# Kernel optimization log

Measured on AMD Instinct MI355X. Metric: run time of the kernel, lower is better.

Reference implementation:

```python
import jax, jax.numpy as jnp
import numpy as np

B, S, D, H = 2, 2048, 1024, 16
DK = D // H

def setup_inputs() -> dict:
    key = jax.random.key(0)
    ks = jax.random.split(key, 11)
    scale = 0.02
    inp = {
        "Q": jax.random.normal(ks[0], (B, S, D), jnp.float32),
        "K": jax.random.normal(ks[1], (B, S, D), jnp.float32),
        "V": jax.random.normal(ks[2], (B, S, D), jnp.float32),
        "mask": jnp.ones((B, S), jnp.int32),
        "Wq": jax.random.normal(ks[3], (D, D), jnp.float32) * scale,
        "bq": jnp.zeros((D,), jnp.float32),
        "Wk": jax.random.normal(ks[4], (D, D), jnp.float32) * scale,
        "bk": jnp.zeros((D,), jnp.float32),
        "Wv": jax.random.normal(ks[5], (D, D), jnp.float32) * scale,
        "bv": jnp.zeros((D,), jnp.float32),
        "Wo": jax.random.normal(ks[6], (D, D), jnp.float32) * scale,
        "bo": jnp.zeros((D,), jnp.float32),
    }
    return inp

def _split_heads(x):
    # [B,S,D] -> [B,H,S,DK]
    return x.reshape(B, S, H, DK).transpose(0, 2, 1, 3)

def reference(Q, K, V, mask, Wq, bq, Wk, bk, Wv, bv, Wo, bo):
    q = _split_heads(Q @ Wq.T + bq)
    k = _split_heads(K @ Wk.T + bk)
    v = _split_heads(V @ Wv.T + bv)
    scores = jnp.einsum("bhqd,bhkd->bhqk", q, k) / jnp.sqrt(jnp.float32(DK))
    # 2D padding mask -> [B,1,1,S], mask==0 positions set to -inf
    m = mask[:, None, None, :]
    scores = jnp.where(m == 0, -jnp.inf, scores)
    attn_weights = jax.nn.softmax(scores, axis=-1)  # [B,H,S,S]
    attn_output = jnp.einsum("bhqk,bhkd->bhqd", attn_weights, v)
    attn_output = attn_output.transpose(0, 2, 1, 3).reshape(B, S, D)
    output = attn_output @ Wo.T + bo
    return (output, attn_weights)
```

## Files before the change

kernel.cpp:

```cpp
#include <hip/hip_runtime.h>
#include <stdint.h>

#define DEVINL __device__ __forceinline__

typedef float  f32x4  __attribute__((ext_vector_type(4)));
typedef float  f32x16 __attribute__((ext_vector_type(16)));
typedef short  s16x8  __attribute__((ext_vector_type(8)));
typedef unsigned short u16x4 __attribute__((ext_vector_type(4)));
typedef unsigned short u16x8 __attribute__((ext_vector_type(8)));

static constexpr int S = 2048, D = 1024, H = 16;
static constexpr size_t OUT0 = (size_t)2 * S * D;

DEVINL unsigned short f2bf(float f) {
  union { float f; unsigned u; } v; v.f = f;
  unsigned r = v.u + 0x7FFFu + ((v.u >> 16) & 1u);
  return (unsigned short)(r >> 16);
}

DEVINL unsigned cvt_pk_bf16(float lo, float hi) {
  unsigned r;
  asm("v_cvt_pk_bf16_f32 %0, %1, %2" : "=v"(r) : "v"(lo), "v"(hi));
  return r;
}

DEVINL void perm32swap(unsigned& a, unsigned& b) {
#if __has_builtin(__builtin_amdgcn_permlane32_swap)
  auto r = __builtin_amdgcn_permlane32_swap(a, b, false, false);
  a = r[0]; b = r[1];
#else
  asm volatile("v_permlane32_swap_b32 %0, %1" : "+v"(a), "+v"(b));
#endif
}

DEVINL void gload_lds16(const void* g, void* l) {
  __builtin_amdgcn_global_load_lds(
      (const __attribute__((address_space(1))) unsigned int*)g,
      (__attribute__((address_space(3))) unsigned int*)l, 16, 0, 0);
}

DEVINL void cvt_body(const float* __restrict__ src, unsigned short* __restrict__ dst, int i) {
  const f32x4* s4 = (const f32x4*)src;
  f32x4 a = s4[i * 2], b = s4[i * 2 + 1];
  u16x8 o;
  o[0] = f2bf(a[0]); o[1] = f2bf(a[1]); o[2] = f2bf(a[2]); o[3] = f2bf(a[3]);
  o[4] = f2bf(b[0]); o[5] = f2bf(b[1]); o[6] = f2bf(b[2]); o[7] = f2bf(b[3]);
  ((u16x8*)dst)[i] = o;
}

__global__ __launch_bounds__(256) void k_cvt_all(
    const float* __restrict__ Q, const float* __restrict__ K, const float* __restrict__ V,
    const float* __restrict__ Wq, const float* __restrict__ Wk,
    const float* __restrict__ Wv, const float* __restrict__ Wo,
    unsigned short* __restrict__ Xq, unsigned short* __restrict__ Xk,
    unsigned short* __restrict__ Xv,
    unsigned short* __restrict__ WQ, unsigned short* __restrict__ WK,
    unsigned short* __restrict__ WV, unsigned short* __restrict__ WO) {
  int i = blockIdx.x;
  const float* src; unsigned short* dst; int item;
  if (i < 6144) {
    int z = i >> 11;
    item = (i & 2047) * 256 + threadIdx.x;
    src = z == 0 ? Q : z == 1 ? K : V;
    dst = z == 0 ? Xq : z == 1 ? Xk : Xv;
  } else {
    int j = i - 6144, z = j >> 9;
    item = (j & 511) * 256 + threadIdx.x;
    src = z == 0 ? Wq : z == 1 ? Wk : z == 2 ? Wv : Wo;
    dst = z == 0 ? WQ : z == 1 ? WK : z == 2 ? WV : WO;
  }
  cvt_body(src, dst, item);
}

template <int MODE>
DEVINL void gemm_tile(const unsigned short* __restrict__ A,
                      const unsigned short* __restrict__ Bw,
                      const float* __restrict__ bias, void* __restrict__ Cout,
                      int tileM, int tileN, float scl, char* smem) {
  const int tid = threadIdx.x;
  const int lane = tid & 63, wave = tid >> 6;
  const int wr = wave >> 1, wc = wave & 1;
  const int l15 = lane & 15, l16 = lane >> 4;
  f32x4 acc[4][4] = {};

#pragma unroll
  for (int p = 0; p < 2; ++p) {
    int c = tid + p * 256;
    int row = c >> 2, col = (c & 3) * 8;
    gload_lds16(A + (((size_t)(tileM + row)) << 10) + col, smem + c * 16);
    gload_lds16(Bw + (((size_t)(tileN + row)) << 10) + col, smem + 8192 + c * 16);
  }
  __syncthreads();

  int cur = 0;
  for (int k0 = 0; k0 < 1024; k0 += 32) {
    if (k0 + 32 < 1024) {
      int nxt = (cur ^ 1) * 16384;
#pragma unroll
      for (int p = 0; p < 2; ++p) {
        int c = tid + p * 256;
        int row = c >> 2, col = (c & 3) * 8;
        gload_lds16(A + (((size_t)(tileM + row)) << 10) + k0 + 32 + col, smem + nxt + c * 16);
        gload_lds16(Bw + (((size_t)(tileN + row)) << 10) + k0 + 32 + col, smem + nxt + 8192 + c * 16);
      }
    }
    const unsigned short* As = (const unsigned short*)(smem + cur * 16384);
    const unsigned short* Bs = (const unsigned short*)(smem + cur * 16384 + 8192);
    s16x8 af[4], bf[4];
#pragma unroll
    for (int i = 0; i < 4; ++i)
      af[i] = *(const s16x8*)&As[(wr * 64 + i * 16 + l15) * 32 + l16 * 8];
#pragma unroll
    for (int i = 0; i < 4; ++i)
      bf[i] = *(const s16x8*)&Bs[(wc * 64 + i * 16 + l15) * 32 + l16 * 8];
#pragma unroll
    for (int i = 0; i < 4; ++i)
#pragma unroll
      for (int j = 0; j < 4; ++j)
        acc[i][j] = __builtin_amdgcn_mfma_f32_16x16x32_bf16(af[i], bf[j], acc[i][j], 0, 0, 0);
    __syncthreads();
    cur ^= 1;
  }

  if (MODE == 0) {
    unsigned short* T = (unsigned short*)smem;
#pragma unroll
    for (int i = 0; i < 4; ++i)
#pragma unroll
      for (int j = 0; j < 4; ++j) {
        int n = wc * 64 + j * 16 + l15;
        float bv = bias[tileN + n];
#pragma unroll
        for (int r = 0; r < 4; ++r) {
          int m = wr * 64 + i * 16 + l16 * 4 + r;
          *(unsigned short*)((char*)T + m * 256 + ((n * 2) ^ ((m & 15) << 4))) =
              f2bf((acc[i][j][r] + bv) * scl);
        }
      }
    __syncthreads();
    {
      int mr = tid >> 1, half = tid & 1;
      int m = tileM + mr;
      int b_ = m >> 11, s_ = m & 2047;
      int h_ = ((tileN + half * 64) >> 6);
      unsigned short* dst = (unsigned short*)Cout + ((size_t)(b_ * H + h_) * S + s_) * 64;
#pragma unroll
      for (int k = 0; k < 8; ++k) {
        u16x8 v = *(const u16x8*)((const char*)T + mr * 256 +
                                  ((half * 128 + k * 16) ^ ((mr & 15) << 4)));
        *(u16x8*)(dst + k * 8) = v;
      }
    }
  } else if (MODE == 2) {
    unsigned short* T = (unsigned short*)smem;
#pragma unroll
    for (int i = 0; i < 4; ++i)
#pragma unroll
      for (int j = 0; j < 4; ++j) {
        int n = wc * 64 + j * 16 + l15;
        float bv = bias[tileN + n];
        int m0 = wr * 64 + i * 16 + l16 * 4;
        u16x4 o;
#pragma unroll
        for (int r = 0; r < 4; ++r) o[r] = f2bf(acc[i][j][r] + bv);
        *(u16x4*)((char*)T + n * 256 + ((m0 * 2) ^ ((n & 15) << 4))) = o;
      }
    __syncthreads();
    {
      int n = tid >> 1, mh = tid & 1;
      int d = (tileN + n) & 63, h_ = (tileN + n) >> 6;
      int b_ = tileM >> 11;
      int kt_ = (((tileM & 2047) + mh * 64) >> 6);
      unsigned short* dst = (unsigned short*)Cout + (size_t)(b_ * H + h_) * S * 64 +
                            (size_t)kt_ * 4096 + d * 64;
#pragma unroll
      for (int k = 0; k < 8; ++k) {
        int mc = mh * 64 + k * 8;
        u16x8 v = *(const u16x8*)((const char*)T + n * 256 + ((mc * 2) ^ ((n & 15) << 4)));
        *(u16x8*)(dst + k * 8) = v;
      }
    }
  } else {
#pragma unroll
    for (int i = 0; i < 4; ++i) {
#pragma unroll
      for (int j = 0; j < 4; ++j) {
        int n = tileN + wc * 64 + j * 16 + l15;
        float bv = bias[n];
#pragma unroll
        for (int r = 0; r < 4; ++r) {
          int m = tileM + wr * 64 + i * 16 + l16 * 4 + r;
          ((float*)Cout)[(size_t)m * 1024 + n] = (acc[i][j][r] + bv) * scl;
        }
      }
    }
  }
}

__global__ __launch_bounds__(256) void k_gemm_qkv(
    const unsigned short* __restrict__ Xq, const unsigned short* __restrict__ Xk,
    const unsigned short* __restrict__ Xv,
    const unsigned short* __restrict__ Wq, const unsigned short* __restrict__ Wk,
    const unsigned short* __restrict__ Wv,
    const float* __restrict__ bq, const float* __restrict__ bk, const float* __restrict__ bv,
    unsigned short* __restrict__ oq, unsigned short* __restrict__ ok,
    unsigned short* __restrict__ vt2) {
  __shared__ alignas(16) char smem[32768];
  int flat = (blockIdx.z * 32 + blockIdx.y) * 8 + blockIdx.x;
  int swz = (flat & 7) * 96 + (flat >> 3);
  int z = swz >> 8;
  int rem = swz & 255;
  int ty = rem >> 3, tx = rem & 7;
  if (z == 2) {
    gemm_tile<2>(Xv, Wv, bv, vt2, ty * 128, tx * 128, 1.0f, smem);
  } else {
    const unsigned short* A = z == 0 ? Xq : Xk;
    const unsigned short* W = z == 0 ? Wq : Wk;
    const float* bias = z == 0 ? bq : bk;
    unsigned short* o = z == 0 ? oq : ok;
    gemm_tile<0>(A, W, bias, o, ty * 128, tx * 128, z == 0 ? 0.125f : 1.0f, smem);
  }
}

__global__ __launch_bounds__(256) void k_gemm_out(const unsigned short* __restrict__ A,
                                                  const unsigned short* __restrict__ W,
                                                  const float* __restrict__ bias,
                                                  float* __restrict__ Cout) {
  __shared__ alignas(16) char smem[32768];
  int flat = blockIdx.y * 8 + blockIdx.x;
  int swz = (flat & 7) * 32 + (flat >> 3);
  int ty = swz >> 3, tx = swz & 7;
  gemm_tile<1>(A, W, bias, Cout, ty * 128, tx * 128, 1.0f, smem);
}

__global__ __launch_bounds__(256) void k_attn_fused(const unsigned short* __restrict__ qw,
                                                    const unsigned short* __restrict__ kw,
                                                    const unsigned short* __restrict__ vt2,
                                                    const int* __restrict__ mask,
                                                    unsigned short* __restrict__ aout,
                                                    float* __restrict__ attw) {
  __shared__ alignas(16) char lds[33792];
  float* lsumW = (float*)(lds + 32768);
  float* lsumT = (float*)(lds + 33280);
  float* nl2lW = (float*)(lds + 33536);
  const float LOG2E = 1.44269504f;

  int flat = blockIdx.y * 32 + blockIdx.x;
  int swzb = (flat & 7) * 128 + (flat >> 3);
  const int bh = swzb >> 5, b = bh >> 4, h = bh & 15;
  const int q0 = (swzb & 31) * 64;
  const int tid = threadIdx.x;
  const int lane = tid & 63, w = tid >> 6;
  const int l31 = lane & 31, hi = lane >> 5;
  const int qg = w >> 1, kb = w & 1;

  const unsigned short* kw_bh = kw + (size_t)bh * S * 64;
  const unsigned short* vt_bh = vt2 + (size_t)bh * S * 64;
  const int* mrow = mask + b * S;

  s16x8 qf[4];
  const unsigned short* qbase = qw + ((size_t)bh * S + q0 + qg * 32 + l31) * 64 + hi * 8;
#pragma unroll
  for (int kc = 0; kc < 4; ++kc) qf[kc] = *(const s16x8*)(qbase + kc * 16);

  f32x16 oT0 = {}, oT1 = {};
  float lsum = 0.f;
  const int swv = (l31 & 7) << 4;

#pragma unroll
  for (int p = 0; p < 2; ++p) {
    int c = tid + p * 256, row = c >> 3, cc = (c & 7) ^ (row & 7);
    gload_lds16(kw_bh + (size_t)row * 64 + cc * 8, lds + c * 16);
    gload_lds16(vt_bh + (size_t)row * 64 + cc * 8, lds + 16384 + c * 16);
  }
  __syncthreads();

  int cur = 0;
  for (int t = 0; t < 32; ++t) {
    if (t + 1 < 32) {
      int nt = t + 1;
      int nxt = (cur ^ 1) * 8192;
#pragma unroll
      for (int p = 0; p < 2; ++p) {
        int c = tid + p * 256, row = c >> 3, cc = (c & 7) ^ (row & 7);
        gload_lds16(kw_bh + ((size_t)(nt * 64 + row)) * 64 + cc * 8, lds + nxt + c * 16);
        gload_lds16(vt_bh + (size_t)nt * 4096 + row * 64 + cc * 8, lds + 16384 + nxt + c * 16);
      }
    }
    const char* Kc = lds + cur * 8192;
    const char* Vc = lds + 16384 + cur * 8192;

    const int krow = kb * 32 + l31;
    f32x16 sT = {};
#pragma unroll
    for (int kc = 0; kc < 4; ++kc) {
      s16x8 ka = *(const s16x8*)(Kc + krow * 128 +
                                 ((kc * 32 + hi * 16) ^ ((krow & 7) << 4)));
      sT = __builtin_amdgcn_mfma_f32_32x32x16_bf16(ka, qf[kc], sT, 0, 0, 0);
    }

    int base = t * 64 + kb * 32 + 4 * hi;
    int m[16];
    *(int4*)&m[0]  = *(const int4*)&mrow[base];
    *(int4*)&m[4]  = *(const int4*)&mrow[base + 8];
    *(int4*)&m[8]  = *(const int4*)&mrow[base + 16];
    *(int4*)&m[12] = *(const int4*)&mrow[base + 24];

    float e[16];
#pragma unroll
    for (int r = 0; r < 16; ++r) {
      e[r] = m[r] ? exp2f(sT[r] * LOG2E) : 0.f;
      lsum += e[r];
    }

    unsigned x0 = cvt_pk_bf16(e[0], e[1]),   x1 = cvt_pk_bf16(e[2], e[3]);
    unsigned x2 = cvt_pk_bf16(e[4], e[5]),   x3 = cvt_pk_bf16(e[6], e[7]);
    unsigned x4 = cvt_pk_bf16(e[8], e[9]),   x5 = cvt_pk_bf16(e[10], e[11]);
    unsigned x6 = cvt_pk_bf16(e[12], e[13]), x7 = cvt_pk_bf16(e[14], e[15]);
    perm32swap(x0, x2); perm32swap(x1, x3);
    perm32swap(x4, x6); perm32swap(x5, x7);
    union { unsigned u[4]; s16x8 v; } p0u, p1u;
    p0u.u[0] = x0; p0u.u[1] = x1; p0u.u[2] = x2; p0u.u[3] = x3;
    p1u.u[0] = x4; p1u.u[1] = x5; p1u.u[2] = x6; p1u.u[3] = x7;

    const int ko0 = kb * 64 + hi * 16, ko1 = kb * 64 + 32 + hi * 16;
    const char* Vr0 = Vc + l31 * 128;
    const char* Vr1 = Vc + (32 + l31) * 128;
    s16x8 va;
    va = *(const s16x8*)(Vr0 + (ko0 ^ swv));
    oT0 = __builtin_amdgcn_mfma_f32_32x32x16_bf16(va, p0u.v, oT0, 0, 0, 0);
    va = *(const s16x8*)(Vr0 + (ko1 ^ swv));
    oT0 = __builtin_amdgcn_mfma_f32_32x32x16_bf16(va, p1u.v, oT0, 0, 0, 0);
    va = *(const s16x8*)(Vr1 + (ko0 ^ swv));
    oT1 = __builtin_amdgcn_mfma_f32_32x32x16_bf16(va, p0u.v, oT1, 0, 0, 0);
    va = *(const s16x8*)(Vr1 + (ko1 ^ swv));
    oT1 = __builtin_amdgcn_mfma_f32_32x32x16_bf16(va, p1u.v, oT1, 0, 0, 0);

    __syncthreads();
    cur ^= 1;
  }

  lsum += __shfl_xor(lsum, 32);
  if (hi == 0) lsumW[w * 32 + l31] = lsum;

  const int sqq = (l31 & 15) << 4;
  {
    char* orow = lds + w * 8192 + l31 * 256;
#pragma unroll
    for (int rg = 0; rg < 4; ++rg) {
      f32x4 c0, c1;
#pragma unroll
      for (int j = 0; j < 4; ++j) { c0[j] = oT0[rg * 4 + j]; c1[j] = oT1[rg * 4 + j]; }
      *(f32x4*)(orow + ((rg * 32 + hi * 16) ^ sqq)) = c0;
      *(f32x4*)(orow + ((128 + rg * 32 + hi * 16) ^ sqq)) = c1;
    }
  }
  __syncthreads();

  if (tid < 64) {
    int qg_ = tid >> 5, qq = tid & 31;
    float tot = lsumW[qg_ * 64 + qq] + lsumW[qg_ * 64 + 32 + qq];
    lsumT[tid] = tot;
    nl2lW[tid] = __log2f(tot);
  }
  __syncthreads();

  {
    int q = tid >> 2, dq = tid & 3;
    int qg_ = q >> 5, qq = q & 31;
    float inv = 1.f / lsumT[q];
    int sq = (qq & 15) << 4;
    float s[16] = {};
#pragma unroll
    for (int w2 = 0; w2 < 2; ++w2) {
      const char* prow = lds + (qg_ * 2 + w2) * 8192 + qq * 256;
#pragma unroll
      for (int c = 0; c < 4; ++c) {
        f32x4 a = *(const f32x4*)(prow + ((dq * 64 + c * 16) ^ sq));
#pragma unroll
        for (int j = 0; j < 4; ++j) s[c * 4 + j] += a[j];
      }
    }
    u16x8 ob0, ob1;
#pragma unroll
    for (int j = 0; j < 8; ++j) { ob0[j] = f2bf(s[j] * inv); ob1[j] = f2bf(s[8 + j] * inv); }
    unsigned short* abase = aout + ((size_t)b * S + q0 + q) * D + h * 64 + dq * 16;
    *(u16x8*)abase = ob0;
    *(u16x8*)(abase + 8) = ob1;
  }

  float nl2l[16];
#pragma unroll
  for (int r = 0; r < 16; ++r) nl2l[r] = nl2lW[qg * 32 + (r & 3) + 8 * (r >> 2) + 4 * hi];

  for (int it = 0; it < 32; ++it) {
    int key0 = it * 64 + kb * 32;
    const unsigned short* kbase = kw_bh + (size_t)(key0 + l31) * 64 + hi * 8;
    s16x8 kfr[4];
#pragma unroll
    for (int kc = 0; kc < 4; ++kc) kfr[kc] = *(const s16x8*)(kbase + kc * 16);
    f32x16 dacc = {};
#pragma unroll
    for (int kc = 0; kc < 4; ++kc)
      dacc = __builtin_amdgcn_mfma_f32_32x32x16_bf16(qf[kc], kfr[kc], dacc, 0, 0, 0);

    int key = key0 + l31;
    int mk = mrow[key];
    float* obase = attw + ((size_t)bh * S + q0 + qg * 32) * S + key;
#pragma unroll
    for (int r = 0; r < 16; ++r) {
      int row = (r & 3) + 8 * (r >> 2) + 4 * hi;
      float wv = mk ? exp2f(dacc[r] * LOG2E - nl2l[r]) : 0.f;
      __builtin_nontemporal_store(wv, obase + (size_t)row * S);
    }
  }
}

extern "C" void kernel_launch(void* const* d_in, const int* in_sizes, int n_in,
                              void* d_out, int out_size, void* d_ws, size_t ws_size,
                              hipStream_t stream) {
  (void)in_sizes; (void)n_in; (void)out_size; (void)ws_size;
  const float* Q  = (const float*)d_in[0];
  const float* K  = (const float*)d_in[1];
  const float* V  = (const float*)d_in[2];
  const int* mask = (const int*)d_in[3];
  const float* Wq = (const float*)d_in[4];
  const float* bq = (const float*)d_in[5];
  const float* Wk = (const float*)d_in[6];
  const float* bk = (const float*)d_in[7];
  const float* Wv = (const float*)d_in[8];
  const float* bv = (const float*)d_in[9];
  const float* Wo = (const float*)d_in[10];
  const float* bo = (const float*)d_in[11];

  char* ws = (char*)d_ws;
  unsigned short* Xbf  = (unsigned short*)(ws + 0);
  unsigned short* Wbf  = (unsigned short*)(ws + 25165824);
  unsigned short* qws  = (unsigned short*)(ws + 33554432);
  unsigned short* kws  = (unsigned short*)(ws + 41943040);
  unsigned short* vt2  = (unsigned short*)(ws + 50331648);
  unsigned short* aoutb= (unsigned short*)(ws + 8388608);
  float* out0 = (float*)d_out;
  float* attw = (float*)d_out + OUT0;

  k_cvt_all<<<dim3(8192), dim3(256), 0, stream>>>(
      Q, K, V, Wq, Wk, Wv, Wo,
      Xbf, Xbf + 4194304, Xbf + 8388608,
      Wbf, Wbf + 1048576, Wbf + 2097152, Wbf + 3145728);

  k_gemm_qkv<<<dim3(8, 32, 3), dim3(256), 0, stream>>>(
      Xbf, Xbf + 4194304, Xbf + 8388608,
      Wbf, Wbf + 1048576, Wbf + 2097152,
      bq, bk, bv, qws, kws, vt2);

  k_attn_fused<<<dim3(32, 32), dim3(256), 0, stream>>>(qws, kws, vt2, mask, aoutb, attw);

  k_gemm_out<<<dim3(8, 32), dim3(256), 0, stream>>>(aoutb, Wbf + 3145728, bo, out0);
}
```

Before: 230.4 us.

## Process two query tiles per block, overlapping first tile's weight writes with second's pass

```diff
diff --git a/kernel.cpp b/kernel.cpp
--- a/kernel.cpp
+++ b/kernel.cpp
@@ -233,22 +233,75 @@
   gemm_tile<1>(A, W, bias, Cout, ty * 128, tx * 128, 1.0f, smem);
 }
 
+DEVINL void o_epilogue(char* lds, float* lsumW, float* lsumT, float* nl2l,
+                       const f32x16& oT0, const f32x16& oT1, float lsum,
+                       int tid, int w, int l31, int hi,
+                       unsigned short* __restrict__ aout, int b, int q0base, int h) {
+  lsum += __shfl_xor(lsum, 32);
+  if (hi == 0) lsumW[w * 32 + l31] = lsum;
+  const int sqq = (l31 & 15) << 4;
+  {
+    char* orow = lds + w * 8192 + l31 * 256;
+#pragma unroll
+    for (int rg = 0; rg < 4; ++rg) {
+      f32x4 c0, c1;
+#pragma unroll
+      for (int j = 0; j < 4; ++j) { c0[j] = oT0[rg * 4 + j]; c1[j] = oT1[rg * 4 + j]; }
+      *(f32x4*)(orow + ((rg * 32 + hi * 16) ^ sqq)) = c0;
+      *(f32x4*)(orow + ((128 + rg * 32 + hi * 16) ^ sqq)) = c1;
+    }
+  }
+  __syncthreads();
+  if (tid < 64) {
+    int qg_ = tid >> 5, qq = tid & 31;
+    float tot = lsumW[qg_ * 64 + qq] + lsumW[qg_ * 64 + 32 + qq];
+    lsumT[tid] = tot;
+    nl2l[tid] = __log2f(tot);
+  }
+  __syncthreads();
+  {
+    int q = tid >> 2, dq = tid & 3;
+    int qg_ = q >> 5, qq = q & 31;
+    float inv = 1.f / lsumT[q];
+    int sq = (qq & 15) << 4;
+    float s[16] = {};
+#pragma unroll
+    for (int w2 = 0; w2 < 2; ++w2) {
+      const char* prow = lds + (qg_ * 2 + w2) * 8192 + qq * 256;
+#pragma unroll
+      for (int c = 0; c < 4; ++c) {
+        f32x4 a = *(const f32x4*)(prow + ((dq * 64 + c * 16) ^ sq));
+#pragma unroll
+        for (int j = 0; j < 4; ++j) s[c * 4 + j] += a[j];
+      }
+    }
+    u16x8 ob0, ob1;
+#pragma unroll
+    for (int j = 0; j < 8; ++j) { ob0[j] = f2bf(s[j] * inv); ob1[j] = f2bf(s[8 + j] * inv); }
+    unsigned short* abase = aout + ((size_t)b * S + q0base + q) * D + h * 64 + dq * 16;
+    *(u16x8*)abase = ob0;
+    *(u16x8*)(abase + 8) = ob1;
+  }
+  __syncthreads();
+}
+
 __global__ __launch_bounds__(256) void k_attn_fused(const unsigned short* __restrict__ qw,
                                                     const unsigned short* __restrict__ kw,
                                                     const unsigned short* __restrict__ vt2,
                                                     const int* __restrict__ mask,
                                                     unsigned short* __restrict__ aout,
                                                     float* __restrict__ attw) {
-  __shared__ alignas(16) char lds[33792];
+  __shared__ alignas(16) char lds[34048];
   float* lsumW = (float*)(lds + 32768);
   float* lsumT = (float*)(lds + 33280);
-  float* nl2lW = (float*)(lds + 33536);
+  float* nl2lX = (float*)(lds + 33536);
+  float* nl2lY = (float*)(lds + 33792);
   const float LOG2E = 1.44269504f;
 
-  int flat = blockIdx.y * 32 + blockIdx.x;
-  int swzb = (flat & 7) * 128 + (flat >> 3);
-  const int bh = swzb >> 5, b = bh >> 4, h = bh & 15;
-  const int q0 = (swzb & 31) * 64;
+  int flat = blockIdx.y * 16 + blockIdx.x;
+  int swzb = (flat & 7) * 64 + (flat >> 3);
+  const int bh = swzb >> 4, b = bh >> 4, h = bh & 15;
+  const int q0 = (swzb & 15) * 128;
   const int tid = threadIdx.x;
   const int lane = tid & 63, w = tid >> 6;
   const int l31 = lane & 31, hi = lane >> 5;
@@ -258,13 +311,19 @@
   const unsigned short* vt_bh = vt2 + (size_t)bh * S * 64;
   const int* mrow = mask + b * S;
 
-  s16x8 qf[4];
-  const unsigned short* qbase = qw + ((size_t)bh * S + q0 + qg * 32 + l31) * 64 + hi * 8;
-#pragma unroll
-  for (int kc = 0; kc < 4; ++kc) qf[kc] = *(const s16x8*)(qbase + kc * 16);
-
-  f32x16 oT0 = {}, oT1 = {};
-  float lsum = 0.f;
+  s16x8 qfX[4], qfY[4];
+  {
+    const unsigned short* qbX = qw + ((size_t)bh * S + q0 + qg * 32 + l31) * 64 + hi * 8;
+    const unsigned short* qbY = qbX + (size_t)64 * 64;
+#pragma unroll
+    for (int kc = 0; kc < 4; ++kc) {
+      qfX[kc] = *(const s16x8*)(qbX + kc * 16);
+      qfY[kc] = *(const s16x8*)(qbY + kc * 16);
+    }
+  }
+
+  f32x16 oTX0 = {}, oTX1 = {};
+  float lsumX = 0.f;
   const int swv = (l31 & 7) << 4;
 
 #pragma unroll
@@ -278,8 +337,7 @@
   int cur = 0;
   for (int t = 0; t < 32; ++t) {
     if (t + 1 < 32) {
-      int nt = t + 1;
-      int nxt = (cur ^ 1) * 8192;
+      int nt = t + 1, nxt = (cur ^ 1) * 8192;
 #pragma unroll
       for (int p = 0; p < 2; ++p) {
         int c = tid + p * 256, row = c >> 3, cc = (c & 7) ^ (row & 7);
@@ -289,14 +347,13 @@
     }
     const char* Kc = lds + cur * 8192;
     const char* Vc = lds + 16384 + cur * 8192;
-
     const int krow = kb * 32 + l31;
+
     f32x16 sT = {};
 #pragma unroll
     for (int kc = 0; kc < 4; ++kc) {
-      s16x8 ka = *(const s16x8*)(Kc + krow * 128 +
-                                 ((kc * 32 + hi * 16) ^ ((krow & 7) << 4)));
-      sT = __builtin_amdgcn_mfma_f32_32x32x16_bf16(ka, qf[kc], sT, 0, 0, 0);
+      s16x8 ka = *(const s16x8*)(Kc + krow * 128 + ((kc * 32 + hi * 16) ^ ((krow & 7) << 4)));
+      sT = __builtin_amdgcn_mfma_f32_32x32x16_bf16(ka, qfX[kc], sT, 0, 0, 0);
     }
 
     int base = t * 64 + kb * 32 + 4 * hi;
@@ -310,7 +367,7 @@
 #pragma unroll
     for (int r = 0; r < 16; ++r) {
       e[r] = m[r] ? exp2f(sT[r] * LOG2E) : 0.f;
-      lsum += e[r];
+      lsumX += e[r];
     }
 
     unsigned x0 = cvt_pk_bf16(e[0], e[1]),   x1 = cvt_pk_bf16(e[2], e[3]);
@@ -328,70 +385,117 @@
     const char* Vr1 = Vc + (32 + l31) * 128;
     s16x8 va;
     va = *(const s16x8*)(Vr0 + (ko0 ^ swv));
-    oT0 = __builtin_amdgcn_mfma_f32_32x32x16_bf16(va, p0u.v, oT0, 0, 0, 0);
+    oTX0 = __builtin_amdgcn_mfma_f32_32x32x16_bf16(va, p0u.v, oTX0, 0, 0, 0);
     va = *(const s16x8*)(Vr0 + (ko1 ^ swv));
-    oT0 = __builtin_amdgcn_mfma_f32_32x32x16_bf16(va, p1u.v, oT0, 0, 0, 0);
+    oTX0 = __builtin_amdgcn_mfma_f32_32x32x16_bf16(va, p1u.v, oTX0, 0, 0, 0);
     va = *(const s16x8*)(Vr1 + (ko0 ^ swv));
-    oT1 = __builtin_amdgcn_mfma_f32_32x32x16_bf16(va, p0u.v, oT1, 0, 0, 0);
+    oTX1 = __builtin_amdgcn_mfma_f32_32x32x16_bf16(va, p0u.v, oTX1, 0, 0, 0);
     va = *(const s16x8*)(Vr1 + (ko1 ^ swv));
-    oT1 = __builtin_amdgcn_mfma_f32_32x32x16_bf16(va, p1u.v, oT1, 0, 0, 0);
+    oTX1 = __builtin_amdgcn_mfma_f32_32x32x16_bf16(va, p1u.v, oTX1, 0, 0, 0);
 
     __syncthreads();
     cur ^= 1;
   }
-
-  lsum += __shfl_xor(lsum, 32);
-  if (hi == 0) lsumW[w * 32 + l31] = lsum;
-
-  const int sqq = (l31 & 15) << 4;
-  {
-    char* orow = lds + w * 8192 + l31 * 256;
-#pragma unroll
-    for (int rg = 0; rg < 4; ++rg) {
-      f32x4 c0, c1;
-#pragma unroll
-      for (int j = 0; j < 4; ++j) { c0[j] = oT0[rg * 4 + j]; c1[j] = oT1[rg * 4 + j]; }
-      *(f32x4*)(orow + ((rg * 32 + hi * 16) ^ sqq)) = c0;
-      *(f32x4*)(orow + ((128 + rg * 32 + hi * 16) ^ sqq)) = c1;
-    }
+  o_epilogue(lds, lsumW, lsumT, nl2lX, oTX0, oTX1, lsumX, tid, w, l31, hi, aout, b, q0, h);
+
+  float nl2lXr[16];
+#pragma unroll
+  for (int r = 0; r < 16; ++r) nl2lXr[r] = nl2lX[qg * 32 + (r & 3) + 8 * (r >> 2) + 4 * hi];
+
+  f32x16 oTY0 = {}, oTY1 = {};
+  float lsumY = 0.f;
+
+#pragma unroll
+  for (int p = 0; p < 2; ++p) {
+    int c = tid + p * 256, row = c >> 3, cc = (c & 7) ^ (row & 7);
+    gload_lds16(kw_bh + (size_t)row * 64 + cc * 8, lds + c * 16);
+    gload_lds16(vt_bh + (size_t)row * 64 + cc * 8, lds + 16384 + c * 16);
   }
   __syncthreads();
 
-  if (tid < 64) {
-    int qg_ = tid >> 5, qq = tid & 31;
-    float tot = lsumW[qg_ * 64 + qq] + lsumW[qg_ * 64 + 32 + qq];
-    lsumT[tid] = tot;
-    nl2lW[tid] = __log2f(tot);
-  }
-  __syncthreads();
-
-  {
-    int q = tid >> 2, dq = tid & 3;
-    int qg_ = q >> 5, qq = q & 31;
-    float inv = 1.f / lsumT[q];
-    int sq = (qq & 15) << 4;
-    float s[16] = {};
-#pragma unroll
-    for (int w2 = 0; w2 < 2; ++w2) {
-      const char* prow = lds + (qg_ * 2 + w2) * 8192 + qq * 256;
-#pragma unroll
-      for (int c = 0; c < 4; ++c) {
-        f32x4 a = *(const f32x4*)(prow + ((dq * 64 + c * 16) ^ sq));
-#pragma unroll
-        for (int j = 0; j < 4; ++j) s[c * 4 + j] += a[j];
-      }
-    }
-    u16x8 ob0, ob1;
-#pragma unroll
-    for (int j = 0; j < 8; ++j) { ob0[j] = f2bf(s[j] * inv); ob1[j] = f2bf(s[8 + j] * inv); }
-    unsigned short* abase = aout + ((size_t)b * S + q0 + q) * D + h * 64 + dq * 16;
-    *(u16x8*)abase = ob0;
-    *(u16x8*)(abase + 8) = ob1;
-  }
-
-  float nl2l[16];
-#pragma unroll
-  for (int r = 0; r < 16; ++r) nl2l[r] = nl2lW[qg * 32 + (r & 3) + 8 * (r >> 2) + 4 * hi];
+  cur = 0;
+  for (int t = 0; t < 32; ++t) {
+    if (t + 1 < 32) {
+      int nt = t + 1, nxt = (cur ^ 1) * 8192;
+#pragma unroll
+      for (int p = 0; p < 2; ++p) {
+        int c = tid + p * 256, row = c >> 3, cc = (c & 7) ^ (row & 7);
+        gload_lds16(kw_bh + ((size_t)(nt * 64 + row)) * 64 + cc * 8, lds + nxt + c * 16);
+        gload_lds16(vt_bh + (size_t)nt * 4096 + row * 64 + cc * 8, lds + 16384 + nxt + c * 16);
+      }
+    }
+    const char* Kc = lds + cur * 8192;
+    const char* Vc = lds + 16384 + cur * 8192;
+    const int krow = kb * 32 + l31;
+
+    s16x8 ka[4];
+#pragma unroll
+    for (int kc = 0; kc < 4; ++kc)
+      ka[kc] = *(const s16x8*)(Kc + krow * 128 + ((kc * 32 + hi * 16) ^ ((krow & 7) << 4)));
+
+    f32x16 sT = {}, dX = {};
+#pragma unroll
+    for (int kc = 0; kc < 4; ++kc) {
+      sT = __builtin_amdgcn_mfma_f32_32x32x16_bf16(ka[kc], qfY[kc], sT, 0, 0, 0);
+      dX = __builtin_amdgcn_mfma_f32_32x32x16_bf16(qfX[kc], ka[kc], dX, 0, 0, 0);
+    }
+
+    int base = t * 64 + kb * 32 + 4 * hi;
+    int m[16];
+    *(int4*)&m[0]  = *(const int4*)&mrow[base];
+    *(int4*)&m[4]  = *(const int4*)&mrow[base + 8];
+    *(int4*)&m[8]  = *(const int4*)&mrow[base + 16];
+    *(int4*)&m[12] = *(const int4*)&mrow[base + 24];
+    int mk = mrow[t * 64 + kb * 32 + l31];
+
+    {
+      float* obase = attw + ((size_t)bh * S + q0 + qg * 32) * S + t * 64 + kb * 32 + l31;
+#pragma unroll
+      for (int r = 0; r < 16; ++r) {
+        int row = (r & 3) + 8 * (r >> 2) + 4 * hi;
+        float wv = mk ? exp2f(dX[r] * LOG2E - nl2lXr[r]) : 0.f;
+        __builtin_nontemporal_store(wv, obase + (size_t)row * S);
+      }
+    }
+
+    float e[16];
+#pragma unroll
+    for (int r = 0; r < 16; ++r) {
+      e[r] = m[r] ? exp2f(sT[r] * LOG2E) : 0.f;
+      lsumY += e[r];
+    }
+
+    unsigned x0 = cvt_pk_bf16(e[0], e[1]),   x1 = cvt_pk_bf16(e[2], e[3]);
+    unsigned x2 = cvt_pk_bf16(e[4], e[5]),   x3 = cvt_pk_bf16(e[6], e[7]);
+    unsigned x4 = cvt_pk_bf16(e[8], e[9]),   x5 = cvt_pk_bf16(e[10], e[11]);
+    unsigned x6 = cvt_pk_bf16(e[12], e[13]), x7 = cvt_pk_bf16(e[14], e[15]);
+    perm32swap(x0, x2); perm32swap(x1, x3);
+    perm32swap(x4, x6); perm32swap(x5, x7);
+    union { unsigned u[4]; s16x8 v; } p0u, p1u;
+    p0u.u[0] = x0; p0u.u[1] = x1; p0u.u[2] = x2; p0u.u[3] = x3;
+    p1u.u[0] = x4; p1u.u[1] = x5; p1u.u[2] = x6; p1u.u[3] = x7;
+
+    const int ko0 = kb * 64 + hi * 16, ko1 = kb * 64 + 32 + hi * 16;
+    const char* Vr0 = Vc + l31 * 128;
+    const char* Vr1 = Vc + (32 + l31) * 128;
+    s16x8 va;
+    va = *(const s16x8*)(Vr0 + (ko0 ^ swv));
+    oTY0 = __builtin_amdgcn_mfma_f32_32x32x16_bf16(va, p0u.v, oTY0, 0, 0, 0);
+    va = *(const s16x8*)(Vr0 + (ko1 ^ swv));
+    oTY0 = __builtin_amdgcn_mfma_f32_32x32x16_bf16(va, p1u.v, oTY0, 0, 0, 0);
+    va = *(const s16x8*)(Vr1 + (ko0 ^ swv));
+    oTY1 = __builtin_amdgcn_mfma_f32_32x32x16_bf16(va, p0u.v, oTY1, 0, 0, 0);
+    va = *(const s16x8*)(Vr1 + (ko1 ^ swv));
+    oTY1 = __builtin_amdgcn_mfma_f32_32x32x16_bf16(va, p1u.v, oTY1, 0, 0, 0);
+
+    __syncthreads();
+    cur ^= 1;
+  }
+  o_epilogue(lds, lsumW, lsumT, nl2lY, oTY0, oTY1, lsumY, tid, w, l31, hi, aout, b, q0 + 64, h);
+
+  float nl2lYr[16];
+#pragma unroll
+  for (int r = 0; r < 16; ++r) nl2lYr[r] = nl2lY[qg * 32 + (r & 3) + 8 * (r >> 2) + 4 * hi];
 
   for (int it = 0; it < 32; ++it) {
     int key0 = it * 64 + kb * 32;
@@ -402,15 +506,15 @@
     f32x16 dacc = {};
 #pragma unroll
     for (int kc = 0; kc < 4; ++kc)
-      dacc = __builtin_amdgcn_mfma_f32_32x32x16_bf16(qf[kc], kfr[kc], dacc, 0, 0, 0);
+      dacc = __builtin_amdgcn_mfma_f32_32x32x16_bf16(qfY[kc], kfr[kc], dacc, 0, 0, 0);
 
     int key = key0 + l31;
     int mk = mrow[key];
-    float* obase = attw + ((size_t)bh * S + q0 + qg * 32) * S + key;
+    float* obase = attw + ((size_t)bh * S + q0 + 64 + qg * 32) * S + key;
 #pragma unroll
     for (int r = 0; r < 16; ++r) {
       int row = (r & 3) + 8 * (r >> 2) + 4 * hi;
-      float wv = mk ? exp2f(dacc[r] * LOG2E - nl2l[r]) : 0.f;
+      float wv = mk ? exp2f(dacc[r] * LOG2E - nl2lYr[r]) : 0.f;
       __builtin_nontemporal_store(wv, obase + (size_t)row * S);
     }
   }
@@ -453,7 +557,7 @@
       Wbf, Wbf + 1048576, Wbf + 2097152,
       bq, bk, bv, qws, kws, vt2);
 
-  k_attn_fused<<<dim3(32, 32), dim3(256), 0, stream>>>(qws, kws, vt2, mask, aoutb, attw);
+  k_attn_fused<<<dim3(16, 32), dim3(256), 0, stream>>>(qws, kws, vt2, mask, aoutb, attw);
 
   k_gemm_out<<<dim3(8, 32), dim3(256), 0, stream>>>(aoutb, Wbf + 3145728, bo, out0);
 }
```

Result: slower. 270.8 us (+17.5%).
